# Kernel optimization log

Hardware: AMD Instinct MI355X
Metric: run time of the kernel (lower is better)

The kernel has to match this reference:

```python
import jax, jax.numpy as jnp
import numpy as np

UNITS = 512
IN_DIM = 256


def setup_inputs() -> dict:
    key = jax.random.key(0)
    k1, k2, k3 = jax.random.split(key, 3)
    x = jax.random.normal(k1, (128, 512, IN_DIM), dtype=jnp.float32)
    # glorot_uniform for kernel
    lim = float(np.sqrt(6.0 / (IN_DIM + UNITS)))
    kernel = jax.random.uniform(k2, (IN_DIM, UNITS), minval=-lim, maxval=lim, dtype=jnp.float32)
    # orthogonal init for recurrent kernel
    a = jax.random.normal(k3, (UNITS, UNITS), dtype=jnp.float32)
    q, r = jnp.linalg.qr(a)
    recurrent_kernel = q * jnp.sign(jnp.diag(r))[None, :]
    bias = jnp.zeros((UNITS,), dtype=jnp.float32)
    return {"x": x, "kernel": kernel, "recurrent_kernel": recurrent_kernel, "bias": bias}


def reference(x, kernel, recurrent_kernel, bias):
    # h_t = tanh(x_t @ W_x + b + h_{t-1} @ W_h), return full sequence [B, T, U]
    B = x.shape[0]
    # Precompute input projection for all timesteps in one batched GEMM
    xp = jnp.einsum('btf,fu->btu', x, kernel) + bias  # [B, T, U]

    def step(h, xp_t):
        h_new = jnp.tanh(xp_t + h @ recurrent_kernel)
        return h_new, h_new

    h0 = jnp.zeros((B, UNITS), dtype=x.dtype)
    _, ys = jax.lax.scan(step, h0, jnp.swapaxes(xp, 0, 1))  # ys: [T, B, U]
    return jnp.swapaxes(ys, 0, 1)
```

## Files before the change

### kernel.cpp

```cpp
#include <hip/hip_runtime.h>
#include <math.h>


#define SENT 0xFFFFFFFFu
#define ALF(p)    __hip_atomic_load((p), __ATOMIC_RELAXED, __HIP_MEMORY_SCOPE_AGENT)
#define ASF(p, v) __hip_atomic_store((p), (v), __ATOMIC_RELAXED, __HIP_MEMORY_SCOPE_AGENT)
#define FMA4(A, W, H) { (A).x += (H)*(W).x; (A).y += (H)*(W).y; (A).z += (H)*(W).z; (A).w += (H)*(W).w; }

typedef __attribute__((ext_vector_type(8))) short bfrag8;
typedef __attribute__((ext_vector_type(4))) float ffrag4;

__device__ __forceinline__ unsigned pack2bf(float a, float b) {
    unsigned ua = __float_as_uint(a), ub = __float_as_uint(b);
    ua += 0x7FFFu + ((ua >> 16) & 1u);
    ub += 0x7FFFu + ((ub >> 16) & 1u);
    return (ua >> 16) | (ub & 0xFFFF0000u);
}
__device__ __forceinline__ short f2bf(float f) {
    unsigned u = __float_as_uint(f);
    u += 0x7FFFu + ((u >> 16) & 1u);
    return (short)(u >> 16);
}

__global__ __launch_bounds__(256) void xp_gemm_mfma(
    const float* __restrict__ x,
    const float* __restrict__ wx,
    const float* __restrict__ bias,
    float* __restrict__ xp,
    float* __restrict__ out)
{
    __shared__ short Abf[128][40];
    __shared__ short Bbf[64][40];

    const int tid  = threadIdx.x;
    const int lane = tid & 63;
    const int w    = tid >> 6;
    const int n0   = blockIdx.x * 64;
    const int m0   = blockIdx.y * 128;

    {
        const float s1 = __uint_as_float(SENT);
        const float4 sv = make_float4(s1, s1, s1, s1);
        const int r = tid >> 1, hf = (tid & 1) * 32;
        float* op = out + (size_t)(m0 + r) * 512 + n0 + hf;
        #pragma unroll
        for (int i = 0; i < 8; ++i) *(float4*)(op + 4 * i) = sv;
    }

    float bsv[4];
    #pragma unroll
    for (int ct = 0; ct < 4; ++ct) bsv[ct] = bias[n0 + ct * 16 + (lane & 15)];

    ffrag4 acc[2][4];
    #pragma unroll
    for (int i = 0; i < 2; ++i)
        #pragma unroll
        for (int j = 0; j < 4; ++j)
            acc[i][j] = (ffrag4){0.f, 0.f, 0.f, 0.f};

    const int arow  = tid >> 1;
    const int ahalf = (tid & 1) * 16;
    const int bk    = tid >> 3;
    const int bn    = (tid & 7) * 8;

    for (int kt = 0; kt < 8; ++kt) {
        {
            const float* src = x + (size_t)(m0 + arow) * 256 + kt * 32 + ahalf;
            const float4 f0 = *(const float4*)(src + 0);
            const float4 f1 = *(const float4*)(src + 4);
            const float4 f2 = *(const float4*)(src + 8);
            const float4 f3 = *(const float4*)(src + 12);
            unsigned* dst = (unsigned*)&Abf[arow][ahalf];
            dst[0] = pack2bf(f0.x, f0.y); dst[1] = pack2bf(f0.z, f0.w);
            dst[2] = pack2bf(f1.x, f1.y); dst[3] = pack2bf(f1.z, f1.w);
            dst[4] = pack2bf(f2.x, f2.y); dst[5] = pack2bf(f2.z, f2.w);
            dst[6] = pack2bf(f3.x, f3.y); dst[7] = pack2bf(f3.z, f3.w);
        }
        {
            const float* src = wx + (size_t)(kt * 32 + bk) * 512 + n0 + bn;
            const float4 f0 = *(const float4*)(src + 0);
            const float4 f1 = *(const float4*)(src + 4);
            Bbf[bn + 0][bk] = f2bf(f0.x); Bbf[bn + 1][bk] = f2bf(f0.y);
            Bbf[bn + 2][bk] = f2bf(f0.z); Bbf[bn + 3][bk] = f2bf(f0.w);
            Bbf[bn + 4][bk] = f2bf(f1.x); Bbf[bn + 5][bk] = f2bf(f1.y);
            Bbf[bn + 6][bk] = f2bf(f1.z); Bbf[bn + 7][bk] = f2bf(f1.w);
        }
        __syncthreads();

        const int kq = (lane >> 4) * 8;
        const bfrag8 a0 = *(const bfrag8*)&Abf[w * 32 + (lane & 15)][kq];
        const bfrag8 a1 = *(const bfrag8*)&Abf[w * 32 + 16 + (lane & 15)][kq];
        #pragma unroll
        for (int ct = 0; ct < 4; ++ct) {
            const bfrag8 bf = *(const bfrag8*)&Bbf[ct * 16 + (lane & 15)][kq];
            acc[0][ct] = __builtin_amdgcn_mfma_f32_16x16x32_bf16(a0, bf, acc[0][ct], 0, 0, 0);
            acc[1][ct] = __builtin_amdgcn_mfma_f32_16x16x32_bf16(a1, bf, acc[1][ct], 0, 0, 0);
        }
        __syncthreads();
    }

    const int col = lane & 15;
    const int rg  = (lane >> 4) * 4;
    #pragma unroll
    for (int rt = 0; rt < 2; ++rt)
        #pragma unroll
        for (int ct = 0; ct < 4; ++ct)
            #pragma unroll
            for (int r = 0; r < 4; ++r)
                xp[(size_t)(m0 + w * 32 + rt * 16 + rg + r) * 512 + n0 + ct * 16 + col]
                    = acc[rt][ct][r] + bsv[ct];
}

__global__ __launch_bounds__(1024) void rnn_scan4(
    const float* __restrict__ wh,
    const float* __restrict__ xp,
    float* __restrict__ out)
{
    __shared__ float h_lds[2][512];
    __shared__ float red[32][2][128];

    const int tid = threadIdx.x;
    const int us  = blockIdx.x & 3;
    const int bg  = blockIdx.x >> 2;
    const int u0  = us * 128;
    const int g   = tid & 31;
    const int s   = tid >> 5;
    const int kbase = s * 16;
    const size_t seq = 512 * 512;

    const float* wr = &wh[(size_t)kbase * 512 + (u0 + 4 * g)];
    const float4 w0  = *(const float4*)(wr + 0  * 512);
    const float4 w1  = *(const float4*)(wr + 1  * 512);
    const float4 w2  = *(const float4*)(wr + 2  * 512);
    const float4 w3  = *(const float4*)(wr + 3  * 512);
    const float4 w4  = *(const float4*)(wr + 4  * 512);
    const float4 w5  = *(const float4*)(wr + 5  * 512);
    const float4 w6  = *(const float4*)(wr + 6  * 512);
    const float4 w7  = *(const float4*)(wr + 7  * 512);
    const float4 w8  = *(const float4*)(wr + 8  * 512);
    const float4 w9  = *(const float4*)(wr + 9  * 512);
    const float4 w10 = *(const float4*)(wr + 10 * 512);
    const float4 w11 = *(const float4*)(wr + 11 * 512);
    const float4 w12 = *(const float4*)(wr + 12 * 512);
    const float4 w13 = *(const float4*)(wr + 13 * 512);
    const float4 w14 = *(const float4*)(wr + 14 * 512);
    const float4 w15 = *(const float4*)(wr + 15 * 512);

    const int ru = tid & 127;
    const int rb = (tid >> 7) & 1;
    const float* xpp = xp + (size_t)(bg * 2 + rb) * seq + u0 + ru;
    float*       hop = out + (size_t)(bg * 2 + rb) * seq + u0 + ru;

    const int sb   = (tid >= 384) ? 1 : 0;
    const int srem = tid - sb * 384;
    const int shk  = (srem < u0) ? srem : srem + 128;
    const float* pollp = out + (size_t)(bg * 2 + sb) * seq + shk;

    for (int t = 0; t < 512; ++t) {
        float xpv = 0.0f;
        if (tid < 256) xpv = xpp[(size_t)t * 512];

        if (t == 0) {
            ((float*)h_lds)[tid] = 0.0f;
        } else if (tid < 768) {
            const float* p = pollp + (size_t)(t - 1) * 512;
            float v;
            int cnt = 0;
            do {
                v = ALF(p);
                if (__float_as_uint(v) != SENT) break;
                __builtin_amdgcn_s_sleep(1);
            } while (++cnt < (1 << 20));
            h_lds[sb][shk] = v;
        }
        __syncthreads();

        float4 a0 = make_float4(0.f, 0.f, 0.f, 0.f);
        float4 a1 = make_float4(0.f, 0.f, 0.f, 0.f);
        const float* hb0 = &h_lds[0][kbase];
        const float* hb1 = &h_lds[1][kbase];
        #define STEP4(W0, W1, W2, W3, OFF) { \
            const float4 h0 = *(const float4*)(hb0 + (OFF)); \
            const float4 h1 = *(const float4*)(hb1 + (OFF)); \
            FMA4(a0, W0, h0.x) FMA4(a0, W1, h0.y) FMA4(a0, W2, h0.z) FMA4(a0, W3, h0.w) \
            FMA4(a1, W0, h1.x) FMA4(a1, W1, h1.y) FMA4(a1, W2, h1.z) FMA4(a1, W3, h1.w) }
        STEP4(w0,  w1,  w2,  w3,  0)
        STEP4(w4,  w5,  w6,  w7,  4)
        STEP4(w8,  w9,  w10, w11, 8)
        STEP4(w12, w13, w14, w15, 12)
        #undef STEP4

        *(float4*)&red[s][0][4 * g] = a0;
        *(float4*)&red[s][1][4 * g] = a1;
        __syncthreads();

        if (tid < 256) {
            float r = xpv;
            #pragma unroll
            for (int ss = 0; ss < 32; ++ss) r += red[ss][rb][ru];
            const float hn = tanhf(r);
            h_lds[rb][u0 + ru] = hn;
            ASF(hop + (size_t)t * 512, hn);
        }
        __syncthreads();
    }
}

__global__ __launch_bounds__(256) void xp_gemm_plain(
    const float* __restrict__ x, const float* __restrict__ wx,
    const float* __restrict__ bias, float* __restrict__ xp)
{
    __shared__ float As[32][68];
    __shared__ float Bs[32][68];
    const int tid = threadIdx.x;
    const int m0 = blockIdx.y * 64;
    const int n0 = blockIdx.x * 64;
    const int tm = tid / 16;
    const int tn = tid % 16;
    float acc[4][4] = {};
    for (int k0 = 0; k0 < 256; k0 += 32) {
        {
            const int kk = tid % 32, r0 = tid / 32;
            #pragma unroll
            for (int rr = 0; rr < 8; ++rr)
                As[kk][r0 + rr * 8] = x[(size_t)(m0 + r0 + rr * 8) * 256 + (k0 + kk)];
        }
        {
            const int nn = tid % 64, r0 = tid / 64;
            #pragma unroll
            for (int rr = 0; rr < 8; ++rr)
                Bs[r0 + rr * 4][nn] = wx[(size_t)(k0 + r0 + rr * 4) * 512 + (n0 + nn)];
        }
        __syncthreads();
        #pragma unroll
        for (int kk = 0; kk < 32; ++kk) {
            const float4 a = *(const float4*)&As[kk][tm * 4];
            const float4 b = *(const float4*)&Bs[kk][tn * 4];
            const float av[4] = {a.x, a.y, a.z, a.w};
            const float bv[4] = {b.x, b.y, b.z, b.w};
            #pragma unroll
            for (int i = 0; i < 4; ++i)
                #pragma unroll
                for (int j = 0; j < 4; ++j)
                    acc[i][j] += av[i] * bv[j];
        }
        __syncthreads();
    }
    #pragma unroll
    for (int i = 0; i < 4; ++i)
        #pragma unroll
        for (int j = 0; j < 4; ++j)
            xp[(size_t)(m0 + tm * 4 + i) * 512 + (n0 + tn * 4 + j)] =
                acc[i][j] + bias[n0 + tn * 4 + j];
}

__global__ __launch_bounds__(1024, 4) void rnn_scan2(
    const float* __restrict__ wh, float* __restrict__ out)
{
    __shared__ float h_lds[2][512];
    __shared__ float red[8][2][512];
    const int tid = threadIdx.x;
    const int g = tid & 127;
    const int s = tid >> 7;
    const int b = tid >> 9;
    const int u = tid & 511;
    float* seqb = out + (size_t)(2 * blockIdx.x + b) * 512 * 512;
    h_lds[b][u] = 0.0f;
    __syncthreads();
    const float4* __restrict__ whv = (const float4*)wh;
    const int kbase = s * 64;
    for (int t = 0; t < 512; ++t) {
        const float xpv = seqb[(size_t)t * 512 + u];
        float4 a0 = make_float4(0.f, 0.f, 0.f, 0.f);
        float4 a1 = make_float4(0.f, 0.f, 0.f, 0.f);
        #pragma unroll 4
        for (int kk = 0; kk < 64; kk += 4) {
            const int k = kbase + kk;
            const float4 h0 = *(const float4*)&h_lds[0][k];
            const float4 h1 = *(const float4*)&h_lds[1][k];
            const float4 v0 = whv[(k + 0) * 128 + g];
            const float4 v1 = whv[(k + 1) * 128 + g];
            const float4 v2 = whv[(k + 2) * 128 + g];
            const float4 v3 = whv[(k + 3) * 128 + g];
            FMA4(a0, v0, h0.x) FMA4(a0, v1, h0.y) FMA4(a0, v2, h0.z) FMA4(a0, v3, h0.w)
            FMA4(a1, v0, h1.x) FMA4(a1, v1, h1.y) FMA4(a1, v2, h1.z) FMA4(a1, v3, h1.w)
        }
        *(float4*)&red[s][0][4 * g] = a0;
        *(float4*)&red[s][1][4 * g] = a1;
        __syncthreads();
        float r = xpv;
        #pragma unroll
        for (int ss = 0; ss < 8; ++ss) r += red[ss][b][u];
        const float hn = tanhf(r);
        h_lds[b][u] = hn;
        seqb[(size_t)t * 512 + u] = hn;
        __syncthreads();
    }
}

extern "C" void kernel_launch(void* const* d_in, const int* in_sizes, int n_in,
                              void* d_out, int out_size, void* d_ws, size_t ws_size,
                              hipStream_t stream) {
    const float* x    = (const float*)d_in[0];
    const float* wx   = (const float*)d_in[1];
    const float* wh   = (const float*)d_in[2];
    const float* bias = (const float*)d_in[3];
    float* out = (float*)d_out;

    const size_t xp_bytes = (size_t)128 * 512 * 512 * sizeof(float);

    if (d_ws != nullptr && ws_size >= xp_bytes) {
        dim3 gm(512 / 64, 65536 / 128);
        xp_gemm_mfma<<<gm, 256, 0, stream>>>(x, wx, bias, (float*)d_ws, out);
        rnn_scan4<<<256, 1024, 0, stream>>>(wh, (const float*)d_ws, out);
    } else {
        dim3 g1(512 / 64, 65536 / 64);
        xp_gemm_plain<<<g1, 256, 0, stream>>>(x, wx, bias, out);
        rnn_scan2<<<64, 1024, 0, stream>>>(wh, out);
    }
}
```

Baseline: 1.081 ms.

## Replace sentinel polling with per-timestep counter flags in the RNN scan

```diff
diff --git a/kernel.cpp b/kernel.cpp
--- a/kernel.cpp
+++ b/kernel.cpp
@@ -2,7 +2,6 @@
 #include <math.h>
 
 
-#define SENT 0xFFFFFFFFu
 #define ALF(p)    __hip_atomic_load((p), __ATOMIC_RELAXED, __HIP_MEMORY_SCOPE_AGENT)
 #define ASF(p, v) __hip_atomic_store((p), (v), __ATOMIC_RELAXED, __HIP_MEMORY_SCOPE_AGENT)
 #define FMA4(A, W, H) { (A).x += (H)*(W).x; (A).y += (H)*(W).y; (A).z += (H)*(W).z; (A).w += (H)*(W).w; }
@@ -26,8 +25,7 @@
     const float* __restrict__ x,
     const float* __restrict__ wx,
     const float* __restrict__ bias,
-    float* __restrict__ xp,
-    float* __restrict__ out)
+    float* __restrict__ xp)
 {
     __shared__ short Abf[128][40];
     __shared__ short Bbf[64][40];
@@ -37,15 +35,6 @@
     const int w    = tid >> 6;
     const int n0   = blockIdx.x * 64;
     const int m0   = blockIdx.y * 128;
-
-    {
-        const float s1 = __uint_as_float(SENT);
-        const float4 sv = make_float4(s1, s1, s1, s1);
-        const int r = tid >> 1, hf = (tid & 1) * 32;
-        float* op = out + (size_t)(m0 + r) * 512 + n0 + hf;
-        #pragma unroll
-        for (int i = 0; i < 8; ++i) *(float4*)(op + 4 * i) = sv;
-    }
 
     float bsv[4];
     #pragma unroll
@@ -111,10 +100,11 @@
                     = acc[rt][ct][r] + bsv[ct];
 }
 
-__global__ __launch_bounds__(1024) void rnn_scan4(
+__global__ __launch_bounds__(1024) void rnn_scan12(
     const float* __restrict__ wh,
     const float* __restrict__ xp,
-    float* __restrict__ out)
+    float* __restrict__ out,
+    int* __restrict__ flags)
 {
     __shared__ float h_lds[2][512];
     __shared__ float red[32][2][128];
@@ -154,7 +144,9 @@
     const int sb   = (tid >= 384) ? 1 : 0;
     const int srem = tid - sb * 384;
     const int shk  = (srem < u0) ? srem : srem + 128;
-    const float* pollp = out + (size_t)(bg * 2 + sb) * seq + shk;
+    const float* datap = out + (size_t)(bg * 2 + sb) * seq + shk;
+
+    int* myflag = flags + bg * 512;
 
     for (int t = 0; t < 512; ++t) {
         float xpv = 0.0f;
@@ -162,16 +154,21 @@
 
         if (t == 0) {
             ((float*)h_lds)[tid] = 0.0f;
-        } else if (tid < 768) {
-            const float* p = pollp + (size_t)(t - 1) * 512;
-            float v;
-            int cnt = 0;
-            do {
-                v = ALF(p);
-                if (__float_as_uint(v) != SENT) break;
-                __builtin_amdgcn_s_sleep(1);
-            } while (++cnt < (1 << 20));
-            h_lds[sb][shk] = v;
+        } else {
+            if (tid < 64) {
+                const int* fp = &myflag[t - 1];
+                int v = ALF(fp);
+                int cnt = 0;
+                while (v < 4 && ++cnt < (1 << 22)) {
+                    __builtin_amdgcn_s_sleep(1);
+                    v = ALF(fp);
+                }
+            }
+            __syncthreads();
+
+            if (tid < 768) {
+                h_lds[sb][shk] = ALF(datap + (size_t)(t - 1) * 512);
+            }
         }
         __syncthreads();
 
@@ -203,6 +200,9 @@
             ASF(hop + (size_t)t * 512, hn);
         }
         __syncthreads();
+        if (tid == 0)
+            __hip_atomic_fetch_add(&myflag[t], 1,
+                                   __ATOMIC_RELAXED, __HIP_MEMORY_SCOPE_AGENT);
     }
 }
 
@@ -307,12 +307,15 @@
     const float* bias = (const float*)d_in[3];
     float* out = (float*)d_out;
 
-    const size_t xp_bytes = (size_t)128 * 512 * 512 * sizeof(float);
-
-    if (d_ws != nullptr && ws_size >= xp_bytes) {
+    const size_t xp_bytes   = (size_t)128 * 512 * 512 * sizeof(float);
+    const size_t flag_bytes = 64 * 512 * sizeof(int);
+
+    if (d_ws != nullptr && ws_size >= xp_bytes + flag_bytes) {
+        int* flags = (int*)((char*)d_ws + xp_bytes);
+        hipMemsetAsync(flags, 0, flag_bytes, stream);
         dim3 gm(512 / 64, 65536 / 128);
-        xp_gemm_mfma<<<gm, 256, 0, stream>>>(x, wx, bias, (float*)d_ws, out);
-        rnn_scan4<<<256, 1024, 0, stream>>>(wh, (const float*)d_ws, out);
+        xp_gemm_mfma<<<gm, 256, 0, stream>>>(x, wx, bias, (float*)d_ws);
+        rnn_scan12<<<256, 1024, 0, stream>>>(wh, (const float*)d_ws, out, flags);
     } else {
         dim3 g1(512 / 64, 65536 / 64);
         xp_gemm_plain<<<g1, 256, 0, stream>>>(x, wx, bias, out);
```

Measured after the change: 1.179 ms. 1.09x slower.
